# Kernel tuning notes

Hardware: AMD Instinct MI355X
Metric: run time of the kernel (lower is better)

The kernel has to match this reference:

```python
import jax, jax.numpy as jnp
import numpy as np

H, BOTTLENECK, TOPK = 2048, 64, 128
TAU, EPS = 1.0, 1e-20

def setup_inputs() -> dict:
    key = jax.random.key(0)
    ks = jax.random.split(key, 7)
    B, T = 4, 4096
    x = jax.random.normal(ks[0], (B, T, H), dtype=jnp.float32)
    Wd = jax.random.normal(ks[1], (H, BOTTLENECK), dtype=jnp.float32) / np.sqrt(H)
    bd = jax.random.normal(ks[2], (BOTTLENECK,), dtype=jnp.float32) * 0.01
    Wu = jax.random.normal(ks[3], (BOTTLENECK, H), dtype=jnp.float32) / np.sqrt(BOTTLENECK)
    bu = jax.random.normal(ks[4], (H,), dtype=jnp.float32) * 0.01
    Wg = jax.random.normal(ks[5], (H,), dtype=jnp.float32) / np.sqrt(H)
    bg = jax.random.normal(ks[6], (), dtype=jnp.float32) * 0.01
    return {"x": x, "Wd": Wd, "bd": bd, "Wu": Wu, "bu": bu, "Wg": Wg, "bg": bg}

def reference(x, Wd, bd, Wu, bu, Wg, bg):
    B, T, _ = x.shape
    k = max(1, min(T, TOPK))
    # gate logits: Linear(H,1).squeeze(-1) -> [B, T]
    logits = jnp.einsum('bth,h->bt', x, Wg) + bg
    # gumbel noise (fixed key for determinism; non-differentiated like torch)
    U = jax.random.uniform(jax.random.key(42), logits.shape, dtype=logits.dtype)
    g = -jnp.log(-jnp.log(U + EPS) + EPS)
    probs = jax.nn.softmax((logits + g) / TAU, axis=-1)            # [B, T]
    topk_idx = jax.lax.top_k(logits, k)[1]                          # [B, k]
    hard = jnp.zeros_like(logits).at[jnp.arange(B)[:, None], topk_idx].set(1.0)
    mask = jax.lax.stop_gradient(hard - probs) + probs              # straight-through
    # bottleneck adapter
    delta = jnp.maximum(x @ Wd + bd, 0.0) @ Wu + bu                 # [B, T, H]
    return x + delta * mask[..., None]
```

## Files before the change

### kernel.cpp

```cpp
#include <hip/hip_runtime.h>
#include <hip/hip_bf16.h>

#define H 2048
#define BN 64
#define TT 4096
#define BB 4
#define KK 128
#define CP_BLOCKS 2048
#define RPB 8

typedef float vf4 __attribute__((ext_vector_type(4)));

__global__ __launch_bounds__(256, 8) void copy_logits_kernel(
    const float* __restrict__ x, const float* __restrict__ Wg,
    float* __restrict__ out, float* __restrict__ lpart, int nhalf) {
    const int lane = threadIdx.x & 63;
    const int wv   = (blockIdx.x * 256 + threadIdx.x) >> 6;
    const int nw   = CP_BLOCKS * 4;
    const vf4* w4 = (const vf4*)Wg + (size_t)(wv & 1) * 256;
    vf4 w[4];
#pragma unroll
    for (int i = 0; i < 4; ++i) w[i] = w4[lane + 64 * i];

    for (int hr = wv; hr < nhalf; hr += nw) {
        const vf4* xs = (const vf4*)x + (size_t)hr * 256;
        vf4*       os = (vf4*)out + (size_t)hr * 256;
        vf4 a[4];
#pragma unroll
        for (int i = 0; i < 4; ++i) a[i] = xs[lane + 64 * i];
        float s0 = 0.f, s1 = 0.f, s2 = 0.f, s3 = 0.f;
#pragma unroll
        for (int i = 0; i < 4; ++i) {
            __builtin_nontemporal_store(a[i], &os[lane + 64 * i]);
            s0 = fmaf(a[i].x, w[i].x, s0);
            s1 = fmaf(a[i].y, w[i].y, s1);
            s2 = fmaf(a[i].z, w[i].z, s2);
            s3 = fmaf(a[i].w, w[i].w, s3);
        }
        float acc = (s0 + s1) + (s2 + s3);
#pragma unroll
        for (int off = 32; off > 0; off >>= 1) acc += __shfl_down(acc, off);
        if (lane == 0) lpart[hr] = acc;
    }
}

__global__ __launch_bounds__(256) void topk_idx_kernel(
    const float* __restrict__ lpart, int* __restrict__ idxlist) {
    __shared__ unsigned keys[TT];
    __shared__ int wsum[4];
    __shared__ int gtp[256], eqp[256];
    const int tid = threadIdx.x;
    const int b   = blockIdx.x;
    const float* lp = lpart + (size_t)b * TT * 2;

    for (int i = tid; i < TT; i += 256) {
        float v = lp[2 * i] + lp[2 * i + 1];
        unsigned u = __float_as_uint(v);
        keys[i] = (u & 0x80000000u) ? ~u : (u | 0x80000000u);
    }
    __syncthreads();

    unsigned prefix = 0;
    int k = KK;
    for (int bit = 31; bit >= 0; --bit) {
        unsigned ref = (prefix >> bit) | 1u;
        int c = 0;
        for (int i = tid; i < TT; i += 256) c += ((keys[i] >> bit) == ref);
#pragma unroll
        for (int off = 32; off > 0; off >>= 1) c += __shfl_down(c, off);
        if ((tid & 63) == 0) wsum[tid >> 6] = c;
        __syncthreads();
        int total = wsum[0] + wsum[1] + wsum[2] + wsum[3];
        __syncthreads();
        if (total >= k) prefix |= (1u << bit);
        else            k -= total;
    }

    const int per = TT / 256, i0 = tid * per, i1 = i0 + per;
    int cgt = 0, ceq = 0;
    for (int i = i0; i < i1; ++i) {
        cgt += (keys[i] > prefix);
        ceq += (keys[i] == prefix);
    }
    gtp[tid] = cgt; eqp[tid] = ceq;
    __syncthreads();
    if (tid == 0) {
        int sg = 0, se = 0;
        for (int t = 0; t < 256; ++t) {
            int a = gtp[t]; gtp[t] = sg; sg += a;
            int c = eqp[t]; eqp[t] = se; se += c;
        }
        wsum[0] = sg;
    }
    __syncthreads();
    const int total_gt = wsum[0];
    const int need_eq  = KK - total_gt;
    int g = gtp[tid], e = eqp[tid];
    int* dst = idxlist + b * KK;
    for (int i = i0; i < i1; ++i) {
        if (keys[i] > prefix)       dst[g++] = b * TT + i;
        else if (keys[i] == prefix) { if (e < need_eq) dst[total_gt + e] = b * TT + i; e++; }
    }
}

__global__ __launch_bounds__(512) void adapter_kernel(
    const float* __restrict__ x, const float* __restrict__ Wd,
    const float* __restrict__ bd, const float* __restrict__ Wu,
    const float* __restrict__ bu, const int* __restrict__ idxlist,
    float* __restrict__ out) {
    __shared__ float hp[8][RPB][BN];
    __shared__ float hs[RPB][BN];
    const int tid  = threadIdx.x;
    const int lane = tid & 63;
    const int g    = tid >> 6;

    int rows[RPB];
#pragma unroll
    for (int r = 0; r < RPB; ++r) rows[r] = idxlist[blockIdx.x * RPB + r];

    float xr[RPB][4];
#pragma unroll
    for (int r = 0; r < RPB; ++r) {
        const float* p = x + (size_t)rows[r] * H + g * 256 + lane;
#pragma unroll
        for (int k = 0; k < 4; ++k) xr[r][k] = p[k * 64];
    }

    float acc[RPB];
#pragma unroll
    for (int r = 0; r < RPB; ++r) acc[r] = 0.f;
    const float* wdp = Wd + (size_t)(g * 256) * BN + lane;
#pragma unroll
    for (int k = 0; k < 4; ++k) {
#pragma unroll 8
        for (int l = 0; l < 64; ++l) {
            float wv = wdp[(size_t)(k * 64 + l) * BN];
#pragma unroll
            for (int r = 0; r < RPB; ++r)
                acc[r] = fmaf(__int_as_float(__builtin_amdgcn_readlane(
                                  __float_as_int(xr[r][k]), l)), wv, acc[r]);
        }
    }
#pragma unroll
    for (int r = 0; r < RPB; ++r) hp[g][r][lane] = acc[r];
    __syncthreads();

    {
        int r = tid >> 6, jj = tid & 63;
        float v = bd[jj];
#pragma unroll
        for (int gg = 0; gg < 8; ++gg) v += hp[gg][r][jj];
        hs[r][jj] = v > 0.f ? v : 0.f;
    }
    __syncthreads();

    const float4* Wu4 = (const float4*)Wu;
    float4 yb = ((const float4*)bu)[tid];
    float4 y[RPB];
#pragma unroll
    for (int r = 0; r < RPB; ++r) y[r] = yb;
    for (int jj = 0; jj < BN; ++jj) {
        float4 wv = Wu4[(size_t)jj * (H / 4) + tid];
#pragma unroll
        for (int r = 0; r < RPB; ++r) {
            float h = hs[r][jj];
            y[r].x = fmaf(h, wv.x, y[r].x); y[r].y = fmaf(h, wv.y, y[r].y);
            y[r].z = fmaf(h, wv.z, y[r].z); y[r].w = fmaf(h, wv.w, y[r].w);
        }
    }
#pragma unroll
    for (int r = 0; r < RPB; ++r) {
        const float4* xr4 = (const float4*)(x + (size_t)rows[r] * H);
        float4*       o4  = (float4*)(out + (size_t)rows[r] * H);
        float4 xa = xr4[tid];
        o4[tid] = make_float4(xa.x + y[r].x, xa.y + y[r].y,
                              xa.z + y[r].z, xa.w + y[r].w);
    }
}

extern "C" void kernel_launch(void* const* d_in, const int* in_sizes, int n_in,
                              void* d_out, int out_size, void* d_ws, size_t ws_size,
                              hipStream_t stream) {
    const float* x  = (const float*)d_in[0];
    const float* Wd = (const float*)d_in[1];
    const float* bd = (const float*)d_in[2];
    const float* Wu = (const float*)d_in[3];
    const float* bu = (const float*)d_in[4];
    const float* Wg = (const float*)d_in[5];
    float* out = (float*)d_out;

    const int nrows = in_sizes[0] / H;
    const int nhalf = nrows * 2;
    float* lpart   = (float*)d_ws;
    int*   idxlist = (int*)((char*)d_ws + (size_t)nhalf * sizeof(float));

    copy_logits_kernel<<<CP_BLOCKS, 256, 0, stream>>>(x, Wg, out, lpart, nhalf);
    topk_idx_kernel<<<BB, 256, 0, stream>>>(lpart, idxlist);
    adapter_kernel<<<(BB * KK) / RPB, 512, 0, stream>>>(x, Wd, bd, Wu, bu, idxlist, out);
}
```

Baseline: 114.9 us.

## Stage x rows through LDS with global_load_lds and process whole rows per wave

The copy/logits kernel now has each wave load a full 2048-float row into LDS using direct global-to-LDS loads, then read it back to store to the output and dot with Wg. Each wave computes a complete row logit, so the partial-sum halves and their recombination in the top-k kernel go away. The grid is halved and the adapter's rows per block drop to 4, which doubles the adapter block count. The LDS staging adds an extra LDS round trip and a full vmcnt wait per row, and Wg is reloaded inside the loop instead of being held in registers.

```diff
diff --git a/kernel.cpp b/kernel.cpp
--- a/kernel.cpp
+++ b/kernel.cpp
@@ -6,56 +6,63 @@
 #define TT 4096
 #define BB 4
 #define KK 128
-#define CP_BLOCKS 2048
-#define RPB 8
+#define CP_BLOCKS 1024
+#define RPB 4
 
 typedef float vf4 __attribute__((ext_vector_type(4)));
 
-__global__ __launch_bounds__(256, 8) void copy_logits_kernel(
+__global__ __launch_bounds__(256) void copy_logits_kernel(
     const float* __restrict__ x, const float* __restrict__ Wg,
-    float* __restrict__ out, float* __restrict__ lpart, int nhalf) {
+    float* __restrict__ out, float* __restrict__ logits, int nrows) {
+    __shared__ char buf[4][8192];
     const int lane = threadIdx.x & 63;
-    const int wv   = (blockIdx.x * 256 + threadIdx.x) >> 6;
-    const int nw   = CP_BLOCKS * 4;
-    const vf4* w4 = (const vf4*)Wg + (size_t)(wv & 1) * 256;
-    vf4 w[4];
-#pragma unroll
-    for (int i = 0; i < 4; ++i) w[i] = w4[lane + 64 * i];
-
-    for (int hr = wv; hr < nhalf; hr += nw) {
-        const vf4* xs = (const vf4*)x + (size_t)hr * 256;
-        vf4*       os = (vf4*)out + (size_t)hr * 256;
-        vf4 a[4];
-#pragma unroll
-        for (int i = 0; i < 4; ++i) a[i] = xs[lane + 64 * i];
+    const int wid  = threadIdx.x >> 6;
+    char* bw = buf[wid];
+    const int wv = blockIdx.x * 4 + wid;
+    const vf4* w4 = (const vf4*)Wg;
+
+    for (int row = wv; row < nrows; row += CP_BLOCKS * 4) {
+        const float* xr = x + ((size_t)row << 11);
+#pragma unroll
+        for (int i = 0; i < 8; ++i) {
+            __builtin_amdgcn_global_load_lds(
+                (const __attribute__((address_space(1))) void*)(xr + ((i << 6) + lane) * 4),
+                (__attribute__((address_space(3))) void*)(bw + i * 1024),
+                16, 0, 0);
+        }
+        asm volatile("s_waitcnt vmcnt(0)" ::: "memory");
+
+        const vf4* bv = (const vf4*)bw;
+        vf4* orow = (vf4*)(out + ((size_t)row << 11));
         float s0 = 0.f, s1 = 0.f, s2 = 0.f, s3 = 0.f;
 #pragma unroll
-        for (int i = 0; i < 4; ++i) {
-            __builtin_nontemporal_store(a[i], &os[lane + 64 * i]);
-            s0 = fmaf(a[i].x, w[i].x, s0);
-            s1 = fmaf(a[i].y, w[i].y, s1);
-            s2 = fmaf(a[i].z, w[i].z, s2);
-            s3 = fmaf(a[i].w, w[i].w, s3);
+        for (int i = 0; i < 8; ++i) {
+            vf4 a  = bv[(i << 6) + lane];
+            vf4 wv4 = w4[(i << 6) + lane];
+            __builtin_nontemporal_store(a, &orow[(i << 6) + lane]);
+            s0 = fmaf(a.x, wv4.x, s0);
+            s1 = fmaf(a.y, wv4.y, s1);
+            s2 = fmaf(a.z, wv4.z, s2);
+            s3 = fmaf(a.w, wv4.w, s3);
         }
         float acc = (s0 + s1) + (s2 + s3);
 #pragma unroll
         for (int off = 32; off > 0; off >>= 1) acc += __shfl_down(acc, off);
-        if (lane == 0) lpart[hr] = acc;
+        if (lane == 0) logits[row] = acc;
     }
 }
 
 __global__ __launch_bounds__(256) void topk_idx_kernel(
-    const float* __restrict__ lpart, int* __restrict__ idxlist) {
+    const float* __restrict__ logits, int* __restrict__ idxlist) {
     __shared__ unsigned keys[TT];
     __shared__ int wsum[4];
     __shared__ int gtp[256], eqp[256];
     const int tid = threadIdx.x;
     const int b   = blockIdx.x;
-    const float* lp = lpart + (size_t)b * TT * 2;
+    const float* lr = logits + (size_t)b * TT;
 
     for (int i = tid; i < TT; i += 256) {
-        float v = lp[2 * i] + lp[2 * i + 1];
-        unsigned u = __float_as_uint(v);
+        unsigned u = __float_as_uint(lr[i]);
         keys[i] = (u & 0x80000000u) ? ~u : (u | 0x80000000u);
     }
     __syncthreads();
@@ -145,7 +152,7 @@
     for (int r = 0; r < RPB; ++r) hp[g][r][lane] = acc[r];
     __syncthreads();
 
-    {
+    if (tid < RPB * BN) {
         int r = tid >> 6, jj = tid & 63;
         float v = bd[jj];
 #pragma unroll
@@ -190,11 +197,10 @@
     float* out = (float*)d_out;
 
     const int nrows = in_sizes[0] / H;
-    const int nhalf = nrows * 2;
-    float* lpart   = (float*)d_ws;
-    int*   idxlist = (int*)((char*)d_ws + (size_t)nhalf * sizeof(float));
-
-    copy_logits_kernel<<<CP_BLOCKS, 256, 0, stream>>>(x, Wg, out, lpart, nhalf);
-    topk_idx_kernel<<<BB, 256, 0, stream>>>(lpart, idxlist);
+    float* logits  = (float*)d_ws;
+    int*   idxlist = (int*)((char*)d_ws + (size_t)nrows * sizeof(float));
+
+    copy_logits_kernel<<<CP_BLOCKS, 256, 0, stream>>>(x, Wg, out, logits, nrows);
+    topk_idx_kernel<<<BB, 256, 0, stream>>>(logits, idxlist);
     adapter_kernel<<<(BB * KK) / RPB, 512, 0, stream>>>(x, Wd, bd, Wu, bu, idxlist, out);
 }
```

New measurement: 98.12 us. 14.6% less time.

## Unroll copy kernel over two half-rows with nontemporal loads; halve adapter rows per block

Applied to the files above, without the earlier changes.

The copy+logits kernel now processes two half-rows per iteration, issuing both sets of loads before the stores and using nontemporal loads. This gives more memory-level parallelism and keeps x from polluting the cache. Wg is reloaded inside the loop instead of held in registers. The adapter now handles 4 rows per block instead of 8, doubling block count for better occupancy, and the reduction stage is guarded to only the needed threads. One risk: the paired loop assumes nhalf is a multiple of 2*nw, otherwise hr2 can run past the end.

```diff
diff --git a/kernel.cpp b/kernel.cpp
--- a/kernel.cpp
+++ b/kernel.cpp
@@ -7,7 +7,7 @@
 #define BB 4
 #define KK 128
 #define CP_BLOCKS 2048
-#define RPB 8
+#define RPB 4
 
 typedef float vf4 __attribute__((ext_vector_type(4)));
 
@@ -17,30 +17,45 @@
     const int lane = threadIdx.x & 63;
     const int wv   = (blockIdx.x * 256 + threadIdx.x) >> 6;
     const int nw   = CP_BLOCKS * 4;
-    const vf4* w4 = (const vf4*)Wg + (size_t)(wv & 1) * 256;
-    vf4 w[4];
-#pragma unroll
-    for (int i = 0; i < 4; ++i) w[i] = w4[lane + 64 * i];
-
-    for (int hr = wv; hr < nhalf; hr += nw) {
-        const vf4* xs = (const vf4*)x + (size_t)hr * 256;
-        vf4*       os = (vf4*)out + (size_t)hr * 256;
-        vf4 a[4];
-#pragma unroll
-        for (int i = 0; i < 4; ++i) a[i] = xs[lane + 64 * i];
+    const vf4* w4  = (const vf4*)Wg + (size_t)(wv & 1) * 256;
+
+    for (int hr = wv; hr < nhalf; hr += 2 * nw) {
+        const int hr2 = hr + nw;
+        const vf4* xs0 = (const vf4*)x + (size_t)hr * 256;
+        const vf4* xs1 = (const vf4*)x + (size_t)hr2 * 256;
+        vf4* os0 = (vf4*)out + (size_t)hr * 256;
+        vf4* os1 = (vf4*)out + (size_t)hr2 * 256;
+
+        vf4 a[4], b[4];
+#pragma unroll
+        for (int i = 0; i < 4; ++i) a[i] = __builtin_nontemporal_load(&xs0[lane + 64 * i]);
+#pragma unroll
+        for (int i = 0; i < 4; ++i) b[i] = __builtin_nontemporal_load(&xs1[lane + 64 * i]);
+
         float s0 = 0.f, s1 = 0.f, s2 = 0.f, s3 = 0.f;
+        float t0 = 0.f, t1 = 0.f, t2 = 0.f, t3 = 0.f;
 #pragma unroll
         for (int i = 0; i < 4; ++i) {
-            __builtin_nontemporal_store(a[i], &os[lane + 64 * i]);
-            s0 = fmaf(a[i].x, w[i].x, s0);
-            s1 = fmaf(a[i].y, w[i].y, s1);
-            s2 = fmaf(a[i].z, w[i].z, s2);
-            s3 = fmaf(a[i].w, w[i].w, s3);
-        }
-        float acc = (s0 + s1) + (s2 + s3);
-#pragma unroll
-        for (int off = 32; off > 0; off >>= 1) acc += __shfl_down(acc, off);
-        if (lane == 0) lpart[hr] = acc;
+            vf4 w = w4[lane + 64 * i];
+            __builtin_nontemporal_store(a[i], &os0[lane + 64 * i]);
+            s0 = fmaf(a[i].x, w.x, s0); s1 = fmaf(a[i].y, w.y, s1);
+            s2 = fmaf(a[i].z, w.z, s2); s3 = fmaf(a[i].w, w.w, s3);
+        }
+#pragma unroll
+        for (int i = 0; i < 4; ++i) {
+            vf4 w = w4[lane + 64 * i];
+            __builtin_nontemporal_store(b[i], &os1[lane + 64 * i]);
+            t0 = fmaf(b[i].x, w.x, t0); t1 = fmaf(b[i].y, w.y, t1);
+            t2 = fmaf(b[i].z, w.z, t2); t3 = fmaf(b[i].w, w.w, t3);
+        }
+        float accA = (s0 + s1) + (s2 + s3);
+        float accB = (t0 + t1) + (t2 + t3);
+#pragma unroll
+        for (int off = 32; off > 0; off >>= 1) {
+            accA += __shfl_down(accA, off);
+            accB += __shfl_down(accB, off);
+        }
+        if (lane == 0) { lpart[hr] = accA; lpart[hr2] = accB; }
     }
 }
 
@@ -145,7 +160,7 @@
     for (int r = 0; r < RPB; ++r) hp[g][r][lane] = acc[r];
     __syncthreads();
 
-    {
+    if (tid < RPB * BN) {
         int r = tid >> 6, jj = tid & 63;
         float v = bd[jj];
 #pragma unroll
```

Result: faster. 101.5 us (-11.7%).
